# Optimization experiments

Measured on AMD Instinct MI355X. Metric: run time of the kernel, lower is better.

## Reference

```python
import jax, jax.numpy as jnp
import numpy as np

DIM, CTX_DIM, HEADS, HIDDEN = 1024, 768, 16, 4096
HEAD_DIM = DIM // HEADS
SCALE = HEAD_DIM ** -0.5


def _layernorm(x, w, b, eps=1e-5):
    mu = jnp.mean(x, axis=-1, keepdims=True)
    var = jnp.var(x, axis=-1, keepdims=True)
    return (x - mu) * jax.lax.rsqrt(var + eps) * w + b


def _heads(t):  # [B, L, H*D] -> [B, H, L, D]
    B, L, _ = t.shape
    return t.reshape(B, L, HEADS, HEAD_DIM).transpose(0, 2, 1, 3)


def _merge(t):  # [B, H, L, D] -> [B, L, H*D]
    B, H, L, D = t.shape
    return t.transpose(0, 2, 1, 3).reshape(B, L, H * D)


def _attn(xq, xkv, qw, qb, kw, kb, vw, vb, pw, pb):
    q = _heads(xq @ qw.T + qb)
    k = _heads(xkv @ kw.T + kb)
    v = _heads(xkv @ vw.T + vb)
    scores = jnp.einsum('bhld,bhsd->bhls', q, k) * SCALE
    probs = jax.nn.softmax(scores, axis=-1)
    out = _merge(jnp.einsum('bhls,bhsd->bhld', probs, v))
    return out @ pw.T + pb


def setup_inputs() -> dict:
    key = jax.random.key(0)
    ks = jax.random.split(key, 16)
    s = 0.02
    d = {
        'x': jax.random.normal(ks[0], (4, 2048, DIM), jnp.float32),
        'context': jax.random.normal(ks[1], (4, 77, CTX_DIM), jnp.float32),
        'ln1_w': jnp.ones((DIM,)), 'ln1_b': jnp.zeros((DIM,)),
        'ln2_w': jnp.ones((DIM,)), 'ln2_b': jnp.zeros((DIM,)),
        'ln3_w': jnp.ones((DIM,)), 'ln3_b': jnp.zeros((DIM,)),
        'sa_qw': jax.random.normal(ks[2], (DIM, DIM)) * s, 'sa_qb': jnp.zeros((DIM,)),
        'sa_kw': jax.random.normal(ks[3], (DIM, DIM)) * s, 'sa_kb': jnp.zeros((DIM,)),
        'sa_vw': jax.random.normal(ks[4], (DIM, DIM)) * s, 'sa_vb': jnp.zeros((DIM,)),
        'sa_pw': jax.random.normal(ks[5], (DIM, DIM)) * s, 'sa_pb': jnp.zeros((DIM,)),
        'ca_qw': jax.random.normal(ks[6], (DIM, DIM)) * s, 'ca_qb': jnp.zeros((DIM,)),
        'ca_kw': jax.random.normal(ks[7], (DIM, CTX_DIM)) * s, 'ca_kb': jnp.zeros((DIM,)),
        'ca_vw': jax.random.normal(ks[8], (DIM, CTX_DIM)) * s, 'ca_vb': jnp.zeros((DIM,)),
        'ca_pw': jax.random.normal(ks[9], (DIM, DIM)) * s, 'ca_pb': jnp.zeros((DIM,)),
        'fc1_w': jax.random.normal(ks[10], (HIDDEN, DIM)) * s, 'fc1_b': jnp.zeros((HIDDEN,)),
        'fc2_w': jax.random.normal(ks[11], (DIM, HIDDEN)) * s, 'fc2_b': jnp.zeros((DIM,)),
    }
    return d


def reference(x, context, ln1_w, ln1_b, ln2_w, ln2_b, ln3_w, ln3_b,
              sa_qw, sa_qb, sa_kw, sa_kb, sa_vw, sa_vb, sa_pw, sa_pb,
              ca_qw, ca_qb, ca_kw, ca_kb, ca_vw, ca_vb, ca_pw, ca_pb,
              fc1_w, fc1_b, fc2_w, fc2_b):
    h = _layernorm(x, ln1_w, ln1_b)
    x = x + _attn(h, h, sa_qw, sa_qb, sa_kw, sa_kb, sa_vw, sa_vb, sa_pw, sa_pb)
    h = _layernorm(x, ln2_w, ln2_b)
    x = x + _attn(h, context, ca_qw, ca_qb, ca_kw, ca_kb, ca_vw, ca_vb, ca_pw, ca_pb)
    h = _layernorm(x, ln3_w, ln3_b)
    h = jax.nn.gelu(h @ fc1_w.T + fc1_b, approximate=False)  # torch nn.GELU = exact
    x = x + (h @ fc2_w.T + fc2_b)
    return x
```

## Files before the change

### kernel.cpp

```cpp
#include <hip/hip_runtime.h>
#include <hip/hip_bf16.h>
#include <cstdint>
#include <cstddef>

typedef __attribute__((ext_vector_type(8))) short bf16x8;
typedef __attribute__((ext_vector_type(4))) float f32x4;
typedef __attribute__((ext_vector_type(16))) float f32x16;

__device__ __forceinline__ unsigned short f2bf(float f) {
  union { float f; unsigned u; } c; c.f = f;
  unsigned r = c.u + 0x7FFFu + ((c.u >> 16) & 1u);
  return (unsigned short)(r >> 16);
}

__device__ __forceinline__ unsigned cvtpk(float lo, float hi) {
  unsigned r;
  asm("v_cvt_pk_bf16_f32 %0, %1, %2" : "=v"(r) : "v"(lo), "v"(hi));
  return r;
}

__device__ __forceinline__ float gelu_fast(float v) {
  const float u = v * (0.7978845608f + 0.0356774081f * v * v);
  const float a = fminf(-2.8853900818f * u, 80.0f);
  return v / (1.0f + exp2f(a));
}

__device__ __forceinline__ int xcd_swz(int bid, int nwg) {
  const int cpx = nwg >> 3;
  return (bid & 7) * cpx + (bid >> 3);
}

typedef const __attribute__((address_space(1))) unsigned int* gas_ptr;
typedef __attribute__((address_space(3))) unsigned int* las_ptr;

__device__ __forceinline__ void gload16(const unsigned short* g, unsigned short* l) {
  __builtin_amdgcn_global_load_lds((gas_ptr)g, (las_ptr)l, 16, 0, 0);
}

struct WJ { const float* s; unsigned short* d; int nblk; };
struct WJobs { WJ j[10]; };

__global__ void wconv_k(WJobs jb) {
  const int bid = blockIdx.x;
  int base = 0, ji = -1;
  #pragma unroll
  for (int k = 0; k < 10; ++k) {
    const int nb = jb.j[k].nblk;
    if (ji < 0) { if (bid < base + nb) ji = k; else base += nb; }
  }
  const int i = (bid - base) * 256 + threadIdx.x;
  float4 v = ((const float4*)jb.j[ji].s)[i];
  ushort4 o;
  o.x = f2bf(v.x); o.y = f2bf(v.y); o.z = f2bf(v.z); o.w = f2bf(v.w);
  ((ushort4*)jb.j[ji].d)[i] = o;
}

__global__ void ctxpad_k(const float* __restrict__ ctx, unsigned short* __restrict__ out) {
  int i = blockIdx.x * blockDim.x + threadIdx.x;
  if (i >= 512 * 192) return;
  int r = i / 192, c4 = i % 192;
  int b = r >> 7, s = r & 127;
  ushort4 o = {0, 0, 0, 0};
  if (s < 77) {
    float4 v = ((const float4*)(ctx + (size_t)(b * 77 + s) * 768))[c4];
    o.x = f2bf(v.x); o.y = f2bf(v.y); o.z = f2bf(v.z); o.w = f2bf(v.w);
  }
  ((ushort4*)out)[i] = o;
}

__global__ __launch_bounds__(256)
void ln_k(const float* __restrict__ x, const float* __restrict__ w,
          const float* __restrict__ b, unsigned short* __restrict__ out) {
  int row = blockIdx.x, tid = threadIdx.x;
  float4 v = ((const float4*)(x + (size_t)row * 1024))[tid];
  float s = v.x + v.y + v.z + v.w;
  float s2 = v.x * v.x + v.y * v.y + v.z * v.z + v.w * v.w;
  #pragma unroll
  for (int m = 1; m < 64; m <<= 1) { s += __shfl_xor(s, m); s2 += __shfl_xor(s2, m); }
  __shared__ float ps[4], ps2[4];
  int wv = tid >> 6;
  if ((tid & 63) == 0) { ps[wv] = s; ps2[wv] = s2; }
  __syncthreads();
  s = ps[0] + ps[1] + ps[2] + ps[3];
  s2 = ps2[0] + ps2[1] + ps2[2] + ps2[3];
  float mu = s * (1.0f / 1024.0f);
  float var = s2 * (1.0f / 1024.0f) - mu * mu;
  float rstd = rsqrtf(var + 1e-5f);
  float4 wv4 = ((const float4*)w)[tid];
  float4 bv4 = ((const float4*)b)[tid];
  ushort4 o;
  o.x = f2bf((v.x - mu) * rstd * wv4.x + bv4.x);
  o.y = f2bf((v.y - mu) * rstd * wv4.y + bv4.y);
  o.z = f2bf((v.z - mu) * rstd * wv4.z + bv4.z);
  o.w = f2bf((v.w - mu) * rstd * wv4.w + bv4.w);
  ((ushort4*)(out + (size_t)row * 1024))[tid] = o;
}

#define SG_A(BUF, H, TE)                                                       \
  _Pragma("unroll")                                                            \
  for (int j = 0; j < AHL; ++j)                                                \
    __builtin_amdgcn_global_load_lds(                                          \
        (gas_ptr)(gA + (TE) + (size_t)((H) * (BM / 2) + j * 64) * (size_t)K),  \
        (las_ptr)(lds_all + (BUF) * AELEMS +                                   \
                  (((H) * (BM / 2) + j * 64) + w * 8) * 64),                   \
        16, 0, 0);

#define SG_B(BUF, H, TE)                                                       \
  _Pragma("unroll")                                                            \
  for (int j = 0; j < BHL; ++j)                                                \
    __builtin_amdgcn_global_load_lds(                                          \
        (gas_ptr)(gB + (TE) + (size_t)((H) * (BN / 2) + j * 64) * (size_t)K),  \
        (las_ptr)(lds_all + 2 * AELEMS + (BUF) * BELEMS +                      \
                  (((H) * (BN / 2) + j * 64) + w * 8) * 64),                   \
        16, 0, 0);

#define RD_A(MHh, BUF)                                                         \
  _Pragma("unroll")                                                            \
  for (int i = 0; i < MH; ++i) {                                               \
    const int r = ((MHh) * MH + i) * 32 + wr * 16 + ln;                        \
    _Pragma("unroll")                                                          \
    for (int kc = 0; kc < 2; ++kc)                                             \
      af[i][kc] = *(const bf16x8*)((const char*)lds_all + (BUF) * ABYTES +     \
                    r * 128 + (((kc * 4 + lg) ^ (r & 7)) * 16));               \
  }

#define RD_B(NHh, BUF)                                                         \
  _Pragma("unroll")                                                            \
  for (int i = 0; i < NIH; ++i) {                                              \
    const int ni = (NHh) * NIH + i;                                            \
    const int r = ni * 64 + wcc * 16 + ln;                                     \
    _Pragma("unroll")                                                          \
    for (int kc = 0; kc < 2; ++kc)                                             \
      bfr[ni][kc] = *(const bf16x8*)((const char*)lds_all + 2 * ABYTES +       \
                    (BUF) * BBYTES + r * 128 + (((kc * 4 + lg) ^ (r & 7)) * 16)); \
  }

#define QUAD(MHh, NHh)                                                         \
  __builtin_amdgcn_s_setprio(1);                                               \
  _Pragma("unroll")                                                            \
  for (int kc = 0; kc < 2; ++kc)                                               \
    _Pragma("unroll")                                                          \
    for (int i = 0; i < MH; ++i)                                               \
      _Pragma("unroll")                                                        \
      for (int j2 = 0; j2 < NIH; ++j2) {                                       \
        const int mi = (MHh) * MH + i, ni = (NHh) * NIH + j2;                  \
        if constexpr (SWAP)                                                    \
          acc[mi][ni] = __builtin_amdgcn_mfma_f32_16x16x32_bf16(               \
              bfr[ni][kc], af[i][kc], acc[mi][ni], 0, 0, 0);                   \
        else                                                                   \
          acc[mi][ni] = __builtin_amdgcn_mfma_f32_16x16x32_bf16(               \
              af[i][kc], bfr[ni][kc], acc[mi][ni], 0, 0, 0);                   \
      }                                                                        \
  __builtin_amdgcn_s_setprio(0);

#define VM_TILE()                                                              \
  do { if constexpr (BM == 256) asm volatile("s_waitcnt vmcnt(6)" ::: "memory"); \
       else                     asm volatile("s_waitcnt vmcnt(3)" ::: "memory"); } while (0)

#define TILE(BUF, TE)                                                          \
  {                                                                            \
    const int t = t2 + ((TE) / 64);                                            \
               \
    RD_A(0, BUF) RD_B(0, BUF)                                                  \
    if (t + 1 < NT) { SG_B((BUF) ^ 1, 1, (TE) + 64) }                          \
    QUAD(0, 0)                                                                 \
    __builtin_amdgcn_s_barrier();                                              \
                             \
    RD_B(1, BUF)                                                               \
    if (t + 2 < NT) { SG_A(BUF, 0, (TE) + 128) }                               \
    QUAD(0, 1)                                                                 \
    __builtin_amdgcn_s_barrier();                                              \
                             \
    RD_A(1, BUF)                                                               \
    if (t + 2 < NT) { SG_B(BUF, 0, (TE) + 128) }                               \
    QUAD(1, 0)                                                                 \
    __builtin_amdgcn_s_barrier();                                              \
      \
    if (t + 2 < NT) { SG_A(BUF, 1, (TE) + 128) }                               \
    QUAD(1, 1)                                                                 \
    if (t + 2 < NT) { VM_TILE(); }                                             \
    else            { asm volatile("s_waitcnt vmcnt(0)" ::: "memory"); }       \
    __builtin_amdgcn_s_barrier();                                              \
  }

template<int BM, int BN, int EPI, int SWAP, int MINW>
__global__ __launch_bounds__(512, MINW)
void gemm8(const unsigned short* __restrict__ A, const unsigned short* __restrict__ Bw,
           const float* __restrict__ bias0, const float* __restrict__ bias1,
           const float* __restrict__ res, void* __restrict__ C0, void* __restrict__ C1,
           int M, int N, int K, float scale0, int nsplit, int vtL) {
  (void)M;
  constexpr int MI = BM / 32;
  constexpr int MH = MI / 2;
  constexpr int AHL = BM / 128;
  constexpr int NI = BN / 64;
  constexpr int NIH = NI / 2;
  constexpr int BHL = BN / 128;
  constexpr int AELEMS = BM * 64;
  constexpr int BELEMS = BN * 64;
  constexpr int ABYTES = AELEMS * 2;
  constexpr int BBYTES = BELEMS * 2;
  __shared__ unsigned short lds_all[2 * AELEMS + 2 * BELEMS];

  const int tid = threadIdx.x;
  const int w = tid >> 6, lane = tid & 63;
  const int wr = w >> 2, wcc = w & 3;
  const int ln = lane & 15, lg = lane >> 4;
  const int nbn = N / BN;
  const int bid = xcd_swz(blockIdx.x, gridDim.x);
  const int bm = bid / nbn, bn = bid % nbn;
  const int NT = K >> 6;

  const int crow = tid >> 3;
  const int cslot = (tid & 7) ^ (crow & 7);

  const unsigned short* gA = A + ((size_t)(bm * BM) + crow) * K + cslot * 8;
  const unsigned short* gB = Bw + ((size_t)(bn * BN) + crow) * K + cslot * 8;

  bf16x8 af[MH][2], bfr[NI][2];
  f32x4 acc[MI][NI] = {};

  SG_A(0, 0, 0) SG_B(0, 0, 0) SG_B(0, 1, 0) SG_A(0, 1, 0)
  if (NT > 1) { SG_A(1, 0, 64) SG_B(1, 0, 64) SG_A(1, 1, 64) }
  VM_TILE();
  __builtin_amdgcn_s_barrier();

  for (int t2 = 0; t2 < NT; t2 += 2) {
    TILE(0, 0)
    TILE(1, 64)
    gA += 128; gB += 128;
  }

  const int rowbase = bm * BM + wr * 16;
  const int colbase = bn * BN + wcc * 16;
  if constexpr (EPI == 1) {
    #pragma unroll
    for (int ni = 0; ni < NI; ++ni) {
      const int col = colbase + ni * 64 + ln;
      const float bv = bias0[col];
      const int hh = col >> 6, dd = col & 63;
      #pragma unroll
      for (int mi = 0; mi < MI; ++mi) {
        const int row0 = rowbase + mi * 32 + lg * 4;
        const int bb = row0 / vtL, ss = row0 % vtL;
        ushort4 pk;
        pk.x = f2bf(acc[mi][ni][0] + bv);
        pk.y = f2bf(acc[mi][ni][1] + bv);
        pk.z = f2bf(acc[mi][ni][2] + bv);
        pk.w = f2bf(acc[mi][ni][3] + bv);
        *(ushort4*)((unsigned short*)C0 + ((size_t)((bb * 16 + hh) * 64 + dd)) * vtL + ss) = pk;
      }
    }
  } else {
    #pragma unroll
    for (int ni = 0; ni < NI; ++ni) {
      const int n0 = colbase + ni * 64 + lg * 4;
      const bool lo = (n0 < nsplit);
      const float* bp = lo ? bias0 : bias1;
      const float sc = lo ? scale0 : 1.0f;
      const int nc = lo ? n0 : n0 - nsplit;
      const int ldc = lo ? nsplit : N - nsplit;
      void* Cp = lo ? C0 : C1;
      const float4 b4 = *(const float4*)(bp + nc);
      #pragma unroll
      for (int mi = 0; mi < MI; ++mi) {
        const size_t mrow = (size_t)rowbase + mi * 32 + ln;
        float v0 = acc[mi][ni][0] + b4.x;
        float v1 = acc[mi][ni][1] + b4.y;
        float v2 = acc[mi][ni][2] + b4.z;
        float v3 = acc[mi][ni][3] + b4.w;
        if constexpr (EPI == 0) {
          ushort4 pk;
          pk.x = f2bf(v0 * sc); pk.y = f2bf(v1 * sc);
          pk.z = f2bf(v2 * sc); pk.w = f2bf(v3 * sc);
          *(ushort4*)((unsigned short*)Cp + mrow * ldc + nc) = pk;
        } else if constexpr (EPI == 2) {
          const float4 r4 = *(const float4*)(res + mrow * ldc + nc);
          float4 o4 = { v0 + r4.x, v1 + r4.y, v2 + r4.z, v3 + r4.w };
          *(float4*)((float*)Cp + mrow * ldc + nc) = o4;
        } else {
          ushort4 pk;
          pk.x = f2bf(gelu_fast(v0)); pk.y = f2bf(gelu_fast(v1));
          pk.z = f2bf(gelu_fast(v2)); pk.w = f2bf(gelu_fast(v3));
          *(ushort4*)((unsigned short*)Cp + mrow * ldc + nc) = pk;
        }
      }
    }
  }
}

__global__ __launch_bounds__(256, 4)
void flash_k(const unsigned short* __restrict__ Q, const unsigned short* __restrict__ Kg,
             const unsigned short* __restrict__ VT, unsigned short* __restrict__ O,
             int Lq, int Lkpad, int kvlen) {
  const int qblocks = Lq >> 7;
  const int bid = xcd_swz(blockIdx.x, gridDim.x);
  const int bh = bid / qblocks, qb = bid - bh * qblocks;
  const int b = bh >> 4, h = bh & 15;
  const int tid = threadIdx.x, w = tid >> 6, lane = tid & 63;
  const int l31 = lane & 31, hi = lane >> 5;

  __shared__ unsigned short Ks[2][64 * 64];
  __shared__ unsigned short Vs[2][64 * 64];

  const size_t qrow = (size_t)b * Lq + qb * 128 + w * 32 + l31;
  bf16x8 qf[4];
  #pragma unroll
  for (int ds = 0; ds < 4; ++ds)
    qf[ds] = *(const bf16x8*)(Q + qrow * 1024 + h * 64 + ds * 16 + hi * 8);

  f32x16 oacc[2] = {};
  f32x4 lacc = {};

  const int nst = (kvlen + 63) >> 6;
  const int srow = lane >> 3;
  const int gslot = (lane & 7) ^ srow;

  auto STAGE = [&](int buf, int st) {
    #pragma unroll
    for (int i = 0; i < 2; ++i) {
      const int r = i * 32 + w * 8 + srow;
      gload16(Kg + ((size_t)b * Lkpad + st * 64 + r) * 1024 + h * 64 + gslot * 8,
              &Ks[buf][(i * 32 + w * 8) * 64]);
      gload16(VT + ((size_t)bh * 64 + r) * Lkpad + (size_t)st * 64 + gslot * 8,
              &Vs[buf][(i * 32 + w * 8) * 64]);
    }
  };

  STAGE(0, 0);

  for (int st = 0; st < nst; ++st) {
    const int cur = st & 1;
    __syncthreads();
    if (st + 1 < nst) STAGE(cur ^ 1, st + 1);

    const char* Kb = (const char*)Ks[cur];
    const char* Vb = (const char*)Vs[cur];

    #pragma unroll
    for (int kb = 0; kb < 2; ++kb) {
      f32x16 s = {};
      {
        const int r = kb * 32 + l31;
        const int sw = (r & 7) << 4;
        __builtin_amdgcn_s_setprio(1);
        #pragma unroll
        for (int ds = 0; ds < 4; ++ds) {
          bf16x8 kf = *(const bf16x8*)(Kb + r * 128 + ((ds * 32 + hi * 16) ^ sw));
          s = __builtin_amdgcn_mfma_f32_32x32x16_bf16(kf, qf[ds], s, 0, 0, 0);
        }
        __builtin_amdgcn_s_setprio(0);
      }

      if (st * 64 + 64 > kvlen) {
        const int kbase = st * 64 + kb * 32 + hi * 4;
        #pragma unroll
        for (int r = 0; r < 16; ++r)
          if (kbase + (r & 3) + 8 * (r >> 2) >= kvlen) s[r] = -1e30f;
      }

      #pragma unroll
      for (int r = 0; r < 16; ++r) s[r] = __builtin_amdgcn_exp2f(s[r]);
      #pragma unroll
      for (int rq = 0; rq < 4; ++rq) {
        f32x4 t = { s[rq * 4 + 0], s[rq * 4 + 1], s[rq * 4 + 2], s[rq * 4 + 3] };
        lacc += t;
      }

      bf16x8 pf[2];
      #pragma unroll
      for (int m = 0; m < 2; ++m) {
        unsigned u0 = cvtpk(s[8 * m + 0], s[8 * m + 1]);
        unsigned u1 = cvtpk(s[8 * m + 2], s[8 * m + 3]);
        unsigned u2 = cvtpk(s[8 * m + 4], s[8 * m + 5]);
        unsigned u3 = cvtpk(s[8 * m + 6], s[8 * m + 7]);
        asm volatile("v_permlane32_swap_b32 %0, %1" : "+v"(u0), "+v"(u2));
        asm volatile("v_permlane32_swap_b32 %0, %1" : "+v"(u1), "+v"(u3));
        union { unsigned u[4]; bf16x8 v; } fr;
        fr.u[0] = u0; fr.u[1] = u1; fr.u[2] = u2; fr.u[3] = u3;
        pf[m] = fr.v;
      }

      {
        const int sw2 = (l31 & 7) << 4;
        __builtin_amdgcn_s_setprio(1);
        #pragma unroll
        for (int db = 0; db < 2; ++db) {
          const int r = db * 32 + l31;
          #pragma unroll
          for (int m = 0; m < 2; ++m) {
            bf16x8 vf = *(const bf16x8*)(Vb + r * 128 +
                          ((kb * 64 + m * 32 + hi * 16) ^ sw2));
            oacc[db] = __builtin_amdgcn_mfma_f32_32x32x16_bf16(vf, pf[m], oacc[db], 0, 0, 0);
          }
        }
        __builtin_amdgcn_s_setprio(0);
      }
    }
  }

  float lt = lacc[0] + lacc[1] + lacc[2] + lacc[3];
  lt += __shfl_xor(lt, 32);
  const float inv = 1.0f / lt;
  #pragma unroll
  for (int db = 0; db < 2; ++db)
    #pragma unroll
    for (int rg = 0; rg < 4; ++rg) {
      ushort4 pk;
      pk.x = f2bf(oacc[db][rg * 4 + 0] * inv);
      pk.y = f2bf(oacc[db][rg * 4 + 1] * inv);
      pk.z = f2bf(oacc[db][rg * 4 + 2] * inv);
      pk.w = f2bf(oacc[db][rg * 4 + 3] * inv);
      *(ushort4*)(O + qrow * 1024 + h * 64 + db * 32 + rg * 8 + hi * 4) = pk;
    }
}

extern "C" void kernel_launch(void* const* d_in, const int* in_sizes, int n_in,
                              void* d_out, int out_size, void* d_ws, size_t ws_size,
                              hipStream_t stream) {
  (void)in_sizes; (void)n_in; (void)out_size; (void)ws_size;
  const float* x     = (const float*)d_in[0];
  const float* ctx   = (const float*)d_in[1];
  const float* ln1_w = (const float*)d_in[2];
  const float* ln1_b = (const float*)d_in[3];
  const float* ln2_w = (const float*)d_in[4];
  const float* ln2_b = (const float*)d_in[5];
  const float* ln3_w = (const float*)d_in[6];
  const float* ln3_b = (const float*)d_in[7];
  const float* sa_qw = (const float*)d_in[8];  const float* sa_qb = (const float*)d_in[9];
  const float* sa_kw = (const float*)d_in[10]; const float* sa_kb = (const float*)d_in[11];
  const float* sa_vw = (const float*)d_in[12]; const float* sa_vb = (const float*)d_in[13];
  const float* sa_pw = (const float*)d_in[14]; const float* sa_pb = (const float*)d_in[15];
  const float* ca_qw = (const float*)d_in[16]; const float* ca_qb = (const float*)d_in[17];
  const float* ca_kw = (const float*)d_in[18]; const float* ca_kb = (const float*)d_in[19];
  const float* ca_vw = (const float*)d_in[20]; const float* ca_vb = (const float*)d_in[21];
  const float* ca_pw = (const float*)d_in[22]; const float* ca_pb = (const float*)d_in[23];
  const float* fc1_w = (const float*)d_in[24]; const float* fc1_b = (const float*)d_in[25];
  const float* fc2_w = (const float*)d_in[26]; const float* fc2_b = (const float*)d_in[27];

  char* ws = (char*)d_ws;
  size_t o = 0;
  auto give = [&](size_t bytes) { size_t r = o; o += (bytes + 255) & ~(size_t)255; return r; };
  const size_t SQ = 1048576, SC = 786432, SF = 4194304;
  unsigned short* w_qk  = (unsigned short*)(ws + give(2 * SQ * 2));
  unsigned short* w_v   = (unsigned short*)(ws + give(SQ * 2));
  unsigned short* w_p   = (unsigned short*)(ws + give(SQ * 2));
  unsigned short* w_caq = (unsigned short*)(ws + give(SQ * 2));
  unsigned short* w_cak = (unsigned short*)(ws + give(SC * 2));
  unsigned short* w_cav = (unsigned short*)(ws + give(SC * 2));
  unsigned short* w_cap = (unsigned short*)(ws + give(SQ * 2));
  unsigned short* w_f1  = (unsigned short*)(ws + give(SF * 2));
  unsigned short* w_f2  = (unsigned short*)(ws + give(SF * 2));
  unsigned short* ctxb  = (unsigned short*)(ws + give(512 * 768 * 2));
  unsigned short* hbuf  = (unsigned short*)(ws + give(8192 * 1024 * 2));
  unsigned short* qbuf  = (unsigned short*)(ws + give(8192 * 1024 * 2));
  unsigned short* kbuf  = (unsigned short*)(ws + give(8192 * 1024 * 2));
  unsigned short* vtbuf = (unsigned short*)(ws + give(8192 * 1024 * 2));
  unsigned short* obuf  = (unsigned short*)(ws + give(8192 * 1024 * 2));
  float*          xc    = (float*)(ws + give(8192 * 1024 * 4));
  unsigned short* gbuf  = qbuf;

  const float QSCALE = 0.125f * 1.44269504088896341f;

  WJobs jb;
  jb.j[0] = { sa_qw, w_qk,      (int)(SQ / 1024) };
  jb.j[1] = { sa_kw, w_qk + SQ, (int)(SQ / 1024) };
  jb.j[2] = { sa_vw, w_v,       (int)(SQ / 1024) };
  jb.j[3] = { sa_pw, w_p,       (int)(SQ / 1024) };
  jb.j[4] = { ca_qw, w_caq,     (int)(SQ / 1024) };
  jb.j[5] = { ca_kw, w_cak,     (int)(SC / 1024) };
  jb.j[6] = { ca_vw, w_cav,     (int)(SC / 1024) };
  jb.j[7] = { ca_pw, w_cap,     (int)(SQ / 1024) };
  jb.j[8] = { fc1_w, w_f1,      (int)(SF / 1024) };
  jb.j[9] = { fc2_w, w_f2,      (int)(SF / 1024) };
  int totblk = 0;
  for (int k = 0; k < 10; ++k) totblk += jb.j[k].nblk;

  wconv_k<<<totblk, 256, 0, stream>>>(jb);
  ctxpad_k<<<384, 256, 0, stream>>>(ctx, ctxb);

  ln_k<<<8192, 256, 0, stream>>>(x, ln1_w, ln1_b, hbuf);
  gemm8<256, 256, 0, 1, 2><<<256, 512, 0, stream>>>(hbuf, w_qk, sa_qb, sa_kb, nullptr, qbuf, kbuf,
                                                    8192, 2048, 1024, QSCALE, 1024, 0);
  gemm8<128, 128, 1, 0, 4><<<512, 512, 0, stream>>>(hbuf, w_v, sa_vb, nullptr, nullptr, vtbuf, nullptr,
                                                    8192, 1024, 1024, 1.0f, 1024, 2048);
  flash_k<<<1024, 256, 0, stream>>>(qbuf, kbuf, vtbuf, obuf, 2048, 2048, 2048);
  gemm8<128, 128, 2, 1, 4><<<512, 512, 0, stream>>>(obuf, w_p, sa_pb, nullptr, x, xc, nullptr,
                                                    8192, 1024, 1024, 1.0f, 1024, 0);

  ln_k<<<8192, 256, 0, stream>>>(xc, ln2_w, ln2_b, hbuf);
  gemm8<128, 128, 0, 1, 4><<<512, 512, 0, stream>>>(hbuf, w_caq, ca_qb, nullptr, nullptr, qbuf, nullptr,
                                                    8192, 1024, 1024, QSCALE, 1024, 0);
  gemm8<128, 128, 0, 1, 4><<<32, 512, 0, stream>>>(ctxb, w_cak, ca_kb, nullptr, nullptr, kbuf, nullptr,
                                                   512, 1024, 768, 1.0f, 1024, 0);
  gemm8<128, 128, 1, 0, 4><<<32, 512, 0, stream>>>(ctxb, w_cav, ca_vb, nullptr, nullptr, vtbuf, nullptr,
                                                   512, 1024, 768, 1.0f, 1024, 128);
  flash_k<<<1024, 256, 0, stream>>>(qbuf, kbuf, vtbuf, obuf, 2048, 128, 77);
  gemm8<128, 128, 2, 1, 4><<<512, 512, 0, stream>>>(obuf, w_cap, ca_pb, nullptr, xc, xc, nullptr,
                                                    8192, 1024, 1024, 1.0f, 1024, 0);

  ln_k<<<8192, 256, 0, stream>>>(xc, ln3_w, ln3_b, hbuf);
  gemm8<256, 256, 3, 1, 2><<<512, 512, 0, stream>>>(hbuf, w_f1, fc1_b, nullptr, nullptr, gbuf, nullptr,
                                                    8192, 4096, 1024, 1.0f, 4096, 0);
  gemm8<128, 128, 2, 1, 4><<<512, 512, 0, stream>>>(gbuf, w_f2, fc2_b, nullptr, xc, d_out, nullptr,
                                                    8192, 1024, 4096, 1.0f, 1024, 0);
}
```

Baseline: 462.3 us.

## Process two query sub-tiles per wave in flash attention; shrink QK/FC1 GEMM tiles

The flash attention kernel now gives each wave two 32-row query sub-tiles (256 query rows per block), so every K and V fragment read from LDS feeds two MFMAs. The launch is halved and occupancy is lowered to 2 blocks per SM to make room for the extra registers. Separately, the fused QK projection and FC1 GEMMs switch from 256x256 to 128x128 tiles with more blocks. The flash change trades occupancy and register pressure for less LDS traffic per FLOP, while the smaller GEMM tiles give more parallelism but less data reuse per block.

```diff
diff --git a/kernel.cpp b/kernel.cpp
--- a/kernel.cpp
+++ b/kernel.cpp
@@ -160,22 +160,18 @@
 #define TILE(BUF, TE)                                                          \
   {                                                                            \
     const int t = t2 + ((TE) / 64);                                            \
-               \
     RD_A(0, BUF) RD_B(0, BUF)                                                  \
     if (t + 1 < NT) { SG_B((BUF) ^ 1, 1, (TE) + 64) }                          \
     QUAD(0, 0)                                                                 \
     __builtin_amdgcn_s_barrier();                                              \
-                             \
     RD_B(1, BUF)                                                               \
     if (t + 2 < NT) { SG_A(BUF, 0, (TE) + 128) }                               \
     QUAD(0, 1)                                                                 \
     __builtin_amdgcn_s_barrier();                                              \
-                             \
     RD_A(1, BUF)                                                               \
     if (t + 2 < NT) { SG_B(BUF, 0, (TE) + 128) }                               \
     QUAD(1, 0)                                                                 \
     __builtin_amdgcn_s_barrier();                                              \
-      \
     if (t + 2 < NT) { SG_A(BUF, 1, (TE) + 128) }                               \
     QUAD(1, 1)                                                                 \
     if (t + 2 < NT) { VM_TILE(); }                                             \
@@ -289,11 +285,11 @@
   }
 }
 
-__global__ __launch_bounds__(256, 4)
+__global__ __launch_bounds__(256, 2)
 void flash_k(const unsigned short* __restrict__ Q, const unsigned short* __restrict__ Kg,
              const unsigned short* __restrict__ VT, unsigned short* __restrict__ O,
              int Lq, int Lkpad, int kvlen) {
-  const int qblocks = Lq >> 7;
+  const int qblocks = Lq >> 8;
   const int bid = xcd_swz(blockIdx.x, gridDim.x);
   const int bh = bid / qblocks, qb = bid - bh * qblocks;
   const int b = bh >> 4, h = bh & 15;
@@ -303,14 +299,16 @@
   __shared__ unsigned short Ks[2][64 * 64];
   __shared__ unsigned short Vs[2][64 * 64];
 
-  const size_t qrow = (size_t)b * Lq + qb * 128 + w * 32 + l31;
-  bf16x8 qf[4];
+  const size_t qrow0 = (size_t)b * Lq + qb * 256 + w * 64 + l31;
+  bf16x8 qf[2][4];
   #pragma unroll
-  for (int ds = 0; ds < 4; ++ds)
-    qf[ds] = *(const bf16x8*)(Q + qrow * 1024 + h * 64 + ds * 16 + hi * 8);
-
-  f32x16 oacc[2] = {};
-  f32x4 lacc = {};
+  for (int u = 0; u < 2; ++u)
+    #pragma unroll
+    for (int ds = 0; ds < 4; ++ds)
+      qf[u][ds] = *(const bf16x8*)(Q + (qrow0 + u * 32) * 1024 + h * 64 + ds * 16 + hi * 8);
+
+  f32x16 oacc[2][2] = {};
+  f32x4 lacc[2] = {};
 
   const int nst = (kvlen + 63) >> 6;
   const int srow = lane >> 3;
@@ -339,7 +337,7 @@
 
     #pragma unroll
     for (int kb = 0; kb < 2; ++kb) {
-      f32x16 s = {};
+      f32x16 s[2] = {};
       {
         const int r = kb * 32 + l31;
         const int sw = (r & 7) << 4;
@@ -347,7 +345,8 @@
         #pragma unroll
         for (int ds = 0; ds < 4; ++ds) {
           bf16x8 kf = *(const bf16x8*)(Kb + r * 128 + ((ds * 32 + hi * 16) ^ sw));
-          s = __builtin_amdgcn_mfma_f32_32x32x16_bf16(kf, qf[ds], s, 0, 0, 0);
+          s[0] = __builtin_amdgcn_mfma_f32_32x32x16_bf16(kf, qf[0][ds], s[0], 0, 0, 0);
+          s[1] = __builtin_amdgcn_mfma_f32_32x32x16_bf16(kf, qf[1][ds], s[1], 0, 0, 0);
         }
         __builtin_amdgcn_s_setprio(0);
       }
@@ -355,30 +354,34 @@
       if (st * 64 + 64 > kvlen) {
         const int kbase = st * 64 + kb * 32 + hi * 4;
         #pragma unroll
-        for (int r = 0; r < 16; ++r)
-          if (kbase + (r & 3) + 8 * (r >> 2) >= kvlen) s[r] = -1e30f;
-      }
-
+        for (int u = 0; u < 2; ++u)
+          #pragma unroll
+          for (int r = 0; r < 16; ++r)
+            if (kbase + (r & 3) + 8 * (r >> 2) >= kvlen) s[u][r] = -1e30f;
+      }
+
+      bf16x8 pf[2][2];
       #pragma unroll
-      for (int r = 0; r < 16; ++r) s[r] = __builtin_amdgcn_exp2f(s[r]);
-      #pragma unroll
-      for (int rq = 0; rq < 4; ++rq) {
-        f32x4 t = { s[rq * 4 + 0], s[rq * 4 + 1], s[rq * 4 + 2], s[rq * 4 + 3] };
-        lacc += t;
-      }
-
-      bf16x8 pf[2];
-      #pragma unroll
-      for (int m = 0; m < 2; ++m) {
-        unsigned u0 = cvtpk(s[8 * m + 0], s[8 * m + 1]);
-        unsigned u1 = cvtpk(s[8 * m + 2], s[8 * m + 3]);
-        unsigned u2 = cvtpk(s[8 * m + 4], s[8 * m + 5]);
-        unsigned u3 = cvtpk(s[8 * m + 6], s[8 * m + 7]);
-        asm volatile("v_permlane32_swap_b32 %0, %1" : "+v"(u0), "+v"(u2));
-        asm volatile("v_permlane32_swap_b32 %0, %1" : "+v"(u1), "+v"(u3));
-        union { unsigned u[4]; bf16x8 v; } fr;
-        fr.u[0] = u0; fr.u[1] = u1; fr.u[2] = u2; fr.u[3] = u3;
-        pf[m] = fr.v;
+      for (int u = 0; u < 2; ++u) {
+        #pragma unroll
+        for (int r = 0; r < 16; ++r) s[u][r] = __builtin_amdgcn_exp2f(s[u][r]);
+        #pragma unroll
+        for (int rq = 0; rq < 4; ++rq) {
+          f32x4 t = { s[u][rq * 4 + 0], s[u][rq * 4 + 1], s[u][rq * 4 + 2], s[u][rq * 4 + 3] };
+          lacc[u] += t;
+        }
+        #pragma unroll
+        for (int m = 0; m < 2; ++m) {
+          unsigned u0 = cvtpk(s[u][8 * m + 0], s[u][8 * m + 1]);
+          unsigned u1 = cvtpk(s[u][8 * m + 2], s[u][8 * m + 3]);
+          unsigned u2 = cvtpk(s[u][8 * m + 4], s[u][8 * m + 5]);
+          unsigned u3 = cvtpk(s[u][8 * m + 6], s[u][8 * m + 7]);
+          asm volatile("v_permlane32_swap_b32 %0, %1" : "+v"(u0), "+v"(u2));
+          asm volatile("v_permlane32_swap_b32 %0, %1" : "+v"(u1), "+v"(u3));
+          union { unsigned uu[4]; bf16x8 v; } fr;
+          fr.uu[0] = u0; fr.uu[1] = u1; fr.uu[2] = u2; fr.uu[3] = u3;
+          pf[u][m] = fr.v;
+        }
       }
 
       {
@@ -391,7 +394,8 @@
           for (int m = 0; m < 2; ++m) {
             bf16x8 vf = *(const bf16x8*)(Vb + r * 128 +
                           ((kb * 64 + m * 32 + hi * 16) ^ sw2));
-            oacc[db] = __builtin_amdgcn_mfma_f32_32x32x16_bf16(vf, pf[m], oacc[db], 0, 0, 0);
+            oacc[0][db] = __builtin_amdgcn_mfma_f32_32x32x16_bf16(vf, pf[0][m], oacc[0][db], 0, 0, 0);
+            oacc[1][db] = __builtin_amdgcn_mfma_f32_32x32x16_bf16(vf, pf[1][m], oacc[1][db], 0, 0, 0);
           }
         }
         __builtin_amdgcn_s_setprio(0);
@@ -399,20 +403,24 @@
     }
   }
 
-  float lt = lacc[0] + lacc[1] + lacc[2] + lacc[3];
-  lt += __shfl_xor(lt, 32);
-  const float inv = 1.0f / lt;
   #pragma unroll
-  for (int db = 0; db < 2; ++db)
+  for (int u = 0; u < 2; ++u) {
+    float lt = lacc[u][0] + lacc[u][1] + lacc[u][2] + lacc[u][3];
+    lt += __shfl_xor(lt, 32);
+    const float inv = 1.0f / lt;
+    const size_t q = qrow0 + u * 32;
     #pragma unroll
-    for (int rg = 0; rg < 4; ++rg) {
-      ushort4 pk;
-      pk.x = f2bf(oacc[db][rg * 4 + 0] * inv);
-      pk.y = f2bf(oacc[db][rg * 4 + 1] * inv);
-      pk.z = f2bf(oacc[db][rg * 4 + 2] * inv);
-      pk.w = f2bf(oacc[db][rg * 4 + 3] * inv);
-      *(ushort4*)(O + qrow * 1024 + h * 64 + db * 32 + rg * 8 + hi * 4) = pk;
-    }
+    for (int db = 0; db < 2; ++db)
+      #pragma unroll
+      for (int rg = 0; rg < 4; ++rg) {
+        ushort4 pk;
+        pk.x = f2bf(oacc[u][db][rg * 4 + 0] * inv);
+        pk.y = f2bf(oacc[u][db][rg * 4 + 1] * inv);
+        pk.z = f2bf(oacc[u][db][rg * 4 + 2] * inv);
+        pk.w = f2bf(oacc[u][db][rg * 4 + 3] * inv);
+        *(ushort4*)(O + q * 1024 + h * 64 + db * 32 + rg * 8 + hi * 4) = pk;
+      }
+  }
 }
 
 extern "C" void kernel_launch(void* const* d_in, const int* in_sizes, int n_in,
@@ -480,11 +488,11 @@
   ctxpad_k<<<384, 256, 0, stream>>>(ctx, ctxb);
 
   ln_k<<<8192, 256, 0, stream>>>(x, ln1_w, ln1_b, hbuf);
-  gemm8<256, 256, 0, 1, 2><<<256, 512, 0, stream>>>(hbuf, w_qk, sa_qb, sa_kb, nullptr, qbuf, kbuf,
-                                                    8192, 2048, 1024, QSCALE, 1024, 0);
+  gemm8<128, 128, 0, 1, 4><<<1024, 512, 0, stream>>>(hbuf, w_qk, sa_qb, sa_kb, nullptr, qbuf, kbuf,
+                                                     8192, 2048, 1024, QSCALE, 1024, 0);
   gemm8<128, 128, 1, 0, 4><<<512, 512, 0, stream>>>(hbuf, w_v, sa_vb, nullptr, nullptr, vtbuf, nullptr,
                                                     8192, 1024, 1024, 1.0f, 1024, 2048);
-  flash_k<<<1024, 256, 0, stream>>>(qbuf, kbuf, vtbuf, obuf, 2048, 2048, 2048);
+  flash_k<<<512, 256, 0, stream>>>(qbuf, kbuf, vtbuf, obuf, 2048, 2048, 2048);
   gemm8<128, 128, 2, 1, 4><<<512, 512, 0, stream>>>(obuf, w_p, sa_pb, nullptr, x, xc, nullptr,
                                                     8192, 1024, 1024, 1.0f, 1024, 0);
 
@@ -495,13 +503,13 @@
                                                    512, 1024, 768, 1.0f, 1024, 0);
   gemm8<128, 128, 1, 0, 4><<<32, 512, 0, stream>>>(ctxb, w_cav, ca_vb, nullptr, nullptr, vtbuf, nullptr,
                                                    512, 1024, 768, 1.0f, 1024, 128);
-  flash_k<<<1024, 256, 0, stream>>>(qbuf, kbuf, vtbuf, obuf, 2048, 128, 77);
+  flash_k<<<512, 256, 0, stream>>>(qbuf, kbuf, vtbuf, obuf, 2048, 128, 77);
   gemm8<128, 128, 2, 1, 4><<<512, 512, 0, stream>>>(obuf, w_cap, ca_pb, nullptr, xc, xc, nullptr,
                                                     8192, 1024, 1024, 1.0f, 1024, 0);
 
   ln_k<<<8192, 256, 0, stream>>>(xc, ln3_w, ln3_b, hbuf);
-  gemm8<256, 256, 3, 1, 2><<<512, 512, 0, stream>>>(hbuf, w_f1, fc1_b, nullptr, nullptr, gbuf, nullptr,
-                                                    8192, 4096, 1024, 1.0f, 4096, 0);
+  gemm8<128, 128, 3, 1, 4><<<2048, 512, 0, stream>>>(hbuf, w_f1, fc1_b, nullptr, nullptr, gbuf, nullptr,
+                                                     8192, 4096, 1024, 1.0f, 4096, 0);
   gemm8<128, 128, 2, 1, 4><<<512, 512, 0, stream>>>(gbuf, w_f2, fc2_b, nullptr, xc, d_out, nullptr,
                                                     8192, 1024, 4096, 1.0f, 1024, 0);
 }
```

New measurement: 482.1 us. 1.04x slower.
